# Optimization experiments

Hardware: AMD Instinct MI355X
Metric: run time of the kernel (lower is better)

Reference implementation:

```python
import jax, jax.numpy as jnp
import numpy as np
import math

B, K, T = 4, 1024, 2048
OD, H = 128, 8


def setup_inputs() -> dict:
    key = jax.random.key(0)
    ks = jax.random.split(key, 6)
    s_in = 1.0 / math.sqrt(K)
    s_u = 1.0 / math.sqrt(H * OD)
    return {
        "x": jax.random.normal(ks[0], (B, K, T), dtype=jnp.float32),
        "Wk": jax.random.uniform(ks[1], (H * OD, K), minval=-s_in, maxval=s_in, dtype=jnp.float32),
        "Wq": jax.random.uniform(ks[2], (H * OD, K), minval=-s_in, maxval=s_in, dtype=jnp.float32),
        "Wv": jax.random.uniform(ks[3], (H * OD, K), minval=-s_in, maxval=s_in, dtype=jnp.float32),
        "Wu": jax.random.uniform(ks[4], (OD, H * OD), minval=-s_u, maxval=s_u, dtype=jnp.float32),
        "bu": jax.random.uniform(ks[5], (OD,), minval=-s_u, maxval=s_u, dtype=jnp.float32),
    }


def reference(x, Wk, Wq, Wv, Wu, bu):
    b, k, t = x.shape
    # QKV projections: Linear applied over channel dim of channels-first input
    keys = jnp.einsum('bkt,jk->bjt', x, Wk).reshape(b, H, OD, t)
    queries = jnp.einsum('bkt,jk->bjt', x, Wq).reshape(b, H, OD, t)
    values = jnp.einsum('bkt,jk->bjt', x, Wv).reshape(b, H, OD, t)
    # attention scores over time: [b, h, t, t]
    dot = jnp.einsum('bhkt,bhki->bhti', queries, keys) / math.sqrt(OD)
    dot = jax.nn.softmax(dot, axis=-1)
    out = jnp.einsum('bhti,bhki->bhkt', dot, values)  # [b, h, od, t]
    # unify heads: weight (OD, H*OD) viewed as (OD_out=k, H=h, OD=e)
    out = jnp.einsum('bhet,khe->bkt', out, Wu.reshape(OD, H, OD))
    return out + bu[None, :, None]
```

## Files before the change

kernel.cpp:

```cpp
#include <hip/hip_runtime.h>
#include <hip/hip_bf16.h>
#include <type_traits>
#include <utility>

#define DEVINL __device__ __forceinline__

typedef unsigned short u16;
typedef unsigned int   u32;
typedef short  s8v  __attribute__((ext_vector_type(8)));
typedef __bf16 b8v  __attribute__((ext_vector_type(8)));
typedef float  f4v  __attribute__((ext_vector_type(4)));
typedef float  f16v __attribute__((ext_vector_type(16)));
typedef u32    u4v  __attribute__((ext_vector_type(4)));

static constexpr int BB = 4, KD = 1024, TT = 2048, OD = 128, NH = 8;
static constexpr int J2 = 2048;

template<class V, class = void> struct mfma_takes : std::false_type {};
template<class V> struct mfma_takes<V, std::void_t<decltype(
    __builtin_amdgcn_mfma_f32_16x16x32_bf16(std::declval<V>(), std::declval<V>(),
                                            std::declval<f4v>(), 0, 0, 0))>> : std::true_type {};

template<class AV>
DEVINL f4v mfma16(AV a, AV b, f4v c) {
  if constexpr (mfma_takes<AV>::value) {
    return __builtin_amdgcn_mfma_f32_16x16x32_bf16(a, b, c, 0, 0, 0);
  } else {
    return __builtin_amdgcn_mfma_f32_16x16x32_bf16(
        __builtin_bit_cast(b8v, a), __builtin_bit_cast(b8v, b), c, 0, 0, 0);
  }
}

template<class V, class = void> struct mfma32_takes : std::false_type {};
template<class V> struct mfma32_takes<V, std::void_t<decltype(
    __builtin_amdgcn_mfma_f32_32x32x16_bf16(std::declval<V>(), std::declval<V>(),
                                            std::declval<f16v>(), 0, 0, 0))>> : std::true_type {};

template<class AV>
DEVINL f16v mfma32(AV a, AV b, f16v c) {
  if constexpr (mfma32_takes<AV>::value) {
    return __builtin_amdgcn_mfma_f32_32x32x16_bf16(a, b, c, 0, 0, 0);
  } else {
    return __builtin_amdgcn_mfma_f32_32x32x16_bf16(
        __builtin_bit_cast(b8v, a), __builtin_bit_cast(b8v, b), c, 0, 0, 0);
  }
}

DEVINL u16 f2bf(float f) {
  union { float f; u32 u; } v; v.f = f;
  u32 u = v.u;
  return (u16)((u + 0x7fffu + ((u >> 16) & 1u)) >> 16);
}
DEVINL float bf2f(u16 h) { union { u32 u; float f; } v; v.u = ((u32)h) << 16; return v.f; }

DEVINL u32 cvtpk_bf16(float a, float b) {
  u32 r;
  asm("v_cvt_pk_bf16_f32 %0, %1, %2" : "=v"(r) : "v"(a), "v"(b));
  return r;
}

DEVINL void gload_lds16(const void* g, void* l) {
  __builtin_amdgcn_global_load_lds(
      (const __attribute__((address_space(1))) void*)g,
      (__attribute__((address_space(3))) void*)l, 16, 0, 0);
}

__global__ void xpose_split_x(const float* __restrict__ x, u16* __restrict__ xTh) {
  __shared__ float tile[32][33];
  const int b  = blockIdx.z;
  const int k0 = blockIdx.y * 32;
  const int t0 = blockIdx.x * 32;
  const int tx = threadIdx.x;
  const int ty = threadIdx.y;
  const float* xb = x + (size_t)b * KD * TT;
#pragma unroll
  for (int j = 0; j < 4; ++j)
    tile[ty + j * 8][tx] = xb[(size_t)(k0 + ty + j * 8) * TT + t0 + tx];
  __syncthreads();
  u16* oh = xTh + (size_t)b * TT * KD;
#pragma unroll
  for (int j = 0; j < 4; ++j) {
    int t = ty + j * 8;
    float v = tile[tx][t];
    oh[(size_t)(t0 + t) * KD + k0 + tx] = f2bf(v);
  }
}

__global__ void split_weights(const float* __restrict__ Wk, const float* __restrict__ Wq,
                              const float* __restrict__ Wv, const float* __restrict__ Wu,
                              u16* __restrict__ Wkqh, u16* __restrict__ Wvh,
                              u16* __restrict__ Wuh,  u16* __restrict__ Wul,
                              float qscale) {
  int i = blockIdx.x * 256 + threadIdx.x;
  if (i < 1048576) {
    Wkqh[i] = f2bf(Wk[i]);
    Wkqh[1048576 + i] = f2bf(Wq[i] * qscale);
    Wvh[i] = f2bf(Wv[i]);
    if (i < 131072) {
      float v = Wu[i];  u16 hh = f2bf(v);
      Wuh[i] = hh;      Wul[i] = f2bf(v - bf2f(hh));
    }
  }
}

template<int EPI>
__global__ __launch_bounds__(256, 3) void gemm_bt_split(
    const u16* __restrict__ Ahi, const u16* __restrict__ Alo,
    const u16* __restrict__ Bhi, const u16* __restrict__ Blo,
    void* __restrict__ Couth,
    const float* __restrict__ bias,
    int Kdim, int ldc, long strideA, long strideB, long strideC, int npass) {
  __shared__ __align__(16) u16 At[128 * 64];
  __shared__ __align__(16) u16 Bt[128 * 64];
  const int tid = threadIdx.x;
  const int w = tid >> 6, l = tid & 63;
  const int wm = w >> 1, wn = w & 1;
  const int lr = l & 15, lg = l >> 4;
  const int b = blockIdx.z;
  const u16* Ah = Ahi + (size_t)b * strideA;
  const u16* Al = Alo ? Alo + (size_t)b * strideA : nullptr;
  const u16* Bh = Bhi + (size_t)b * strideB;
  const u16* Bl = Blo ? Blo + (size_t)b * strideB : nullptr;
  const int m0 = blockIdx.x * 128;
  const int n0 = (EPI == 3) ? ((blockIdx.y & 15) * 128) : (blockIdx.y * 128);
  const int ky = (EPI == 3) ? (blockIdx.y >> 4) : 0;
  const int kspan = (EPI == 3) ? (Kdim / 2) : Kdim;
  const int kbase = ky * kspan;

  int srow[4], soff[4];
#pragma unroll
  for (int i = 0; i < 4; ++i) {
    int c = tid + i * 256;
    int row = c >> 3, q = c & 7;
    srow[i] = row;
    soff[i] = (q ^ (row & 7)) * 8;
  }

  f4v acc[4][4] = {};

  const int spi = kspan / 64;
  const int iters = npass * spi;
  for (int it = 0; it < iters; ++it) {
    const int seg = it / spi;
    const int k = kbase + (it - seg * spi) * 64;
    const u16* As = (seg == 2 || (seg == 1 && npass == 2)) ? Al : Ah;
    const u16* Bs = (seg == 1 && npass == 3) ? Bl : Bh;
#pragma unroll
    for (int i = 0; i < 4; ++i) {
      int c = tid + i * 256;
      gload_lds16(As + (size_t)(m0 + srow[i]) * Kdim + k + soff[i], (char*)At + c * 16);
      gload_lds16(Bs + (size_t)(n0 + srow[i]) * Kdim + k + soff[i], (char*)Bt + c * 16);
    }
    __syncthreads();
    __builtin_amdgcn_s_setprio(1);
#pragma unroll
    for (int kk = 0; kk < 2; ++kk) {
      const int q = kk * 4 + lg;
      s8v a[4], bb[4];
#pragma unroll
      for (int mi = 0; mi < 4; ++mi) {
        int row = wm * 64 + mi * 16 + lr;
        a[mi] = *(const s8v*)(&At[row * 64 + (q ^ (row & 7)) * 8]);
      }
#pragma unroll
      for (int ni = 0; ni < 4; ++ni) {
        int row = wn * 64 + ni * 16 + lr;
        bb[ni] = *(const s8v*)(&Bt[row * 64 + (q ^ (row & 7)) * 8]);
      }
#pragma unroll
      for (int mi = 0; mi < 4; ++mi)
#pragma unroll
        for (int ni = 0; ni < 4; ++ni)
          acc[mi][ni] = mfma16(a[mi], bb[ni], acc[mi][ni]);
    }
    __builtin_amdgcn_s_setprio(0);
    __syncthreads();
  }

  if constexpr (EPI == 2) {
    u16* Ch = (u16*)Couth + (size_t)b * strideC;
#pragma unroll
    for (int mi = 0; mi < 4; ++mi)
#pragma unroll
      for (int ni = 0; ni < 4; ++ni)
#pragma unroll
        for (int r = 0; r < 4; ++r) {
          int m = m0 + wm * 64 + mi * 16 + lg * 4 + r;
          int n = n0 + wn * 64 + ni * 16 + lr;
          Ch[(size_t)m * ldc + n] = f2bf(acc[mi][ni][r]);
        }
  } else if constexpr (EPI == 3) {
    float* C = (float*)Couth + ((size_t)ky * BB + b) * strideC;
#pragma unroll
    for (int mi = 0; mi < 4; ++mi)
#pragma unroll
      for (int ni = 0; ni < 4; ++ni)
#pragma unroll
        for (int r = 0; r < 4; ++r) {
          int m = m0 + wm * 64 + mi * 16 + lg * 4 + r;
          int n = n0 + wn * 64 + ni * 16 + lr;
          C[(size_t)m * ldc + n] = acc[mi][ni][r];
        }
  } else {
    float* C = (float*)Couth + (size_t)b * strideC;
#pragma unroll
    for (int mi = 0; mi < 4; ++mi)
#pragma unroll
      for (int ni = 0; ni < 4; ++ni)
#pragma unroll
        for (int r = 0; r < 4; ++r) {
          int m = m0 + wm * 64 + mi * 16 + lg * 4 + r;
          int n = n0 + wn * 64 + ni * 16 + lr;
          C[(size_t)m * ldc + n] = acc[mi][ni][r] + bias[m];
        }
  }
}

__global__ void addbias(const float* __restrict__ part, float* __restrict__ out,
                        const float* __restrict__ bias) {
  int i = blockIdx.x * 256 + threadIdx.x;
  f4v a = ((const f4v*)part)[i];
  f4v c = ((const f4v*)part)[i + 262144];
  float bs = bias[(i >> 9) & 127];
  f4v r;
#pragma unroll
  for (int j = 0; j < 4; ++j) r[j] = a[j] + c[j] + bs;
  ((f4v*)out)[i] = r;
}

__global__ __launch_bounds__(256, 2) void attn_fwd(
    const u16* __restrict__ QKTh, const u16* __restrict__ Vh,
    u16* __restrict__ OTh) {
  __shared__ __align__(16) u16 Ksh[2][32 * 128];
  __shared__ __align__(16) u16 Vsh[2][128 * 32];

  const int bid = blockIdx.x;
  const int lid = (bid & 7) * 64 + (bid >> 3);
  const int t0 = (lid & 15) * 128;
  const int h  = (lid >> 4) & 7;
  const int b  = lid >> 7;

  const int tid = threadIdx.x;
  const int w = tid >> 6, l = tid & 63;
  const int lw = l & 31, hi = l >> 5;
  const size_t qb = (size_t)b * TT * J2;
  const u16* Qh_ = QKTh + qb + 1024 + h * 128;
  const u16* Kh_ = QKTh + qb + h * 128;
  const u16* Vh_ = Vh + (size_t)b * 1024 * TT + (size_t)h * 128 * TT;

  int koff[2], kdo[2], voff[2], vdo[2];
#pragma unroll
  for (int i = 0; i < 2; ++i) {
    int c = tid + i * 256;
    { int row = c >> 4, q = c & 15;
      koff[i] = row * J2 + (q ^ (row & 7)) * 8;  kdo[i] = c * 16; }
    { int row = c >> 2, q = c & 3;
      voff[i] = row * TT + (q ^ ((row >> 1) & 3)) * 8;  vdo[i] = c * 16; }
  }

#define ATTN_STAGE(BSEL, I0) do {                                          \
    _Pragma("unroll")                                                      \
    for (int i_ = 0; i_ < 2; ++i_) {                                       \
      gload_lds16(Kh_ + (size_t)(I0) * J2 + koff[i_], (char*)Ksh[BSEL] + kdo[i_]); \
      gload_lds16(Vh_ + voff[i_] + (I0),              (char*)Vsh[BSEL] + vdo[i_]); \
    } } while (0)

  s8v qh[8];
  {
    const size_t trow = (size_t)(t0 + w * 32 + lw) * J2;
#pragma unroll
    for (int st = 0; st < 8; ++st)
      qh[st] = *(const s8v*)(Qh_ + trow + st * 16 + hi * 8);
  }

  f16v o[4] = {};
  float lsum = 0.f;

  ATTN_STAGE(0, 0);

  for (int it = 0; it < 64; ++it) {
    const int cur = it & 1;
    if (it + 1 < 64) {
      ATTN_STAGE(cur ^ 1, (it + 1) * 32);
      asm volatile("s_waitcnt vmcnt(4)" ::: "memory");
    } else {
      asm volatile("s_waitcnt vmcnt(0)" ::: "memory");
    }
    __builtin_amdgcn_s_barrier();

    const u16* Ks = Ksh[cur];
    const u16* Vs = Vsh[cur];
    f16v s = {};
    __builtin_amdgcn_s_setprio(1);
#pragma unroll
    for (int st = 0; st < 8; ++st) {
      s8v kf = *(const s8v*)(&Ks[lw * 128 + (((st * 2 + hi) ^ (lw & 7)) * 8)]);
      s = mfma32(kf, qh[st], s);
    }
    __builtin_amdgcn_s_setprio(0);

    u32 wp[4][2];
    float ps = 0.f;
#pragma unroll
    for (int g = 0; g < 4; ++g) {
      float e0 = exp2f(s[g * 4 + 0]);
      float e1 = exp2f(s[g * 4 + 1]);
      float e2 = exp2f(s[g * 4 + 2]);
      float e3 = exp2f(s[g * 4 + 3]);
      ps += (e0 + e1) + (e2 + e3);
      wp[g][0] = cvtpk_bf16(e0, e1);
      wp[g][1] = cvtpk_bf16(e2, e3);
    }
    lsum += ps;

    s8v pa[2];
#pragma unroll
    for (int ks = 0; ks < 2; ++ks) {
      u32 a0 = wp[2 * ks][0], b0 = wp[2 * ks + 1][0];
      u32 a1 = wp[2 * ks][1], b1 = wp[2 * ks + 1][1];
      asm volatile("v_permlane32_swap_b32 %0, %1" : "+v"(a0), "+v"(b0));
      asm volatile("v_permlane32_swap_b32 %0, %1" : "+v"(a1), "+v"(b1));
      u4v fw; fw[0] = a0; fw[1] = a1; fw[2] = b0; fw[3] = b1;
      pa[ks] = __builtin_bit_cast(s8v, fw);
    }

    __builtin_amdgcn_s_setprio(1);
#pragma unroll
    for (int ks = 0; ks < 2; ++ks) {
#pragma unroll
      for (int et = 0; et < 4; ++et) {
        const int vrow = et * 32 + lw;
        s8v vh = *(const s8v*)(&Vs[vrow * 32 +
                                   (((ks * 2 + hi) ^ ((vrow >> 1) & 3)) * 8)]);
        o[et] = mfma32(pa[ks], vh, o[et]);
      }
    }
    __builtin_amdgcn_s_setprio(0);
    if (it + 1 < 64)
      __builtin_amdgcn_s_barrier();
  }
#undef ATTN_STAGE

  lsum += __shfl_xor(lsum, 32);

  u16* oh = OTh + (size_t)b * TT * 1024;
#pragma unroll
  for (int r = 0; r < 16; ++r) {
    const int qrow = (r & 3) + 8 * (r >> 2) + 4 * hi;
    float ls = __shfl(lsum, qrow);
    float inv = 1.0f / ls;
    int t = t0 + w * 32 + qrow;
#pragma unroll
    for (int et = 0; et < 4; ++et) {
      int he = h * 128 + et * 32 + lw;
      oh[(size_t)t * 1024 + he] = f2bf(o[et][r] * inv);
    }
  }
}

extern "C" void kernel_launch(void* const* d_in, const int* in_sizes, int n_in,
                              void* d_out, int out_size, void* d_ws, size_t ws_size,
                              hipStream_t stream) {
  const float* x  = (const float*)d_in[0];
  const float* Wk = (const float*)d_in[1];
  const float* Wq = (const float*)d_in[2];
  const float* Wv = (const float*)d_in[3];
  const float* Wu = (const float*)d_in[4];
  const float* bu = (const float*)d_in[5];
  float* out = (float*)d_out;

  const size_t need_bytes = 2ull * (8388608ull + 2097152ull + 1048576ull +
                                    131072ull * 2 + 16777216ull + 8388608ull +
                                    8388608ull + 4194304ull);
  if (ws_size < need_bytes) {
    (void)hipMemsetAsync(d_out, 0, (size_t)out_size * sizeof(float), stream);
    return;
  }
  u16* p = (u16*)d_ws;
  u16* xTh = p;  p += 8388608;
  u16* Wkqh = p; p += 2097152;
  u16* Wvh = p;  p += 1048576;
  u16* Wuh = p;  p += 131072;
  u16* Wul = p;  p += 131072;
  u16* QKTh = p; p += 16777216;
  u16* Vh = p;   p += 8388608;
  u16* OTh = p;  p += 8388608;
  float* Cpart = (float*)p; p += 4194304;

  const float qscale = 0.08838834764831845f * 1.4426950408889634f;

  xpose_split_x<<<dim3(64, 32, 4), dim3(32, 8), 0, stream>>>(x, xTh);
  split_weights<<<4096, 256, 0, stream>>>(Wk, Wq, Wv, Wu, Wkqh, Wvh, Wuh, Wul, qscale);

  gemm_bt_split<2><<<dim3(16, 16, 4), 256, 0, stream>>>(
      xTh, nullptr, Wkqh, nullptr, QKTh, nullptr,
      1024, 2048, 2097152L, 0L, 4194304L, 1);
  gemm_bt_split<2><<<dim3(8, 16, 4), 256, 0, stream>>>(
      Wvh, nullptr, xTh, nullptr, Vh, nullptr,
      1024, 2048, 0L, 2097152L, 2097152L, 1);
  attn_fwd<<<dim3(512), dim3(256), 0, stream>>>(QKTh, Vh, OTh);
  gemm_bt_split<3><<<dim3(1, 32, 4), 256, 0, stream>>>(
      Wuh, Wul, OTh, nullptr, Cpart, nullptr,
      1024, 2048, 0L, 2097152L, 262144L, 2);
  addbias<<<1024, 256, 0, stream>>>(Cpart, out, bu);
}
```

Baseline: 187.0 us.

## Software-pipeline attention with 4-deep LDS ring and next-tile QK overlap

Result: no change. 188.3 us (+0.7%).

```diff
diff --git a/kernel.cpp b/kernel.cpp
--- a/kernel.cpp
+++ b/kernel.cpp
@@ -231,8 +231,8 @@
 __global__ __launch_bounds__(256, 2) void attn_fwd(
     const u16* __restrict__ QKTh, const u16* __restrict__ Vh,
     u16* __restrict__ OTh) {
-  __shared__ __align__(16) u16 Ksh[2][32 * 128];
-  __shared__ __align__(16) u16 Vsh[2][128 * 32];
+  __shared__ __align__(16) u16 Ksh[4][32 * 128];
+  __shared__ __align__(16) u16 Vsh[4][128 * 32];
 
   const int bid = blockIdx.x;
   const int lid = (bid & 7) * 64 + (bid >> 3);
@@ -265,6 +265,17 @@
       gload_lds16(Vh_ + voff[i_] + (I0),              (char*)Vsh[BSEL] + vdo[i_]); \
     } } while (0)
 
+#define ATTN_QK(SACC, BSEL) do {                                           \
+    const u16* Ks_ = Ksh[BSEL];                                            \
+    __builtin_amdgcn_s_setprio(1);                                         \
+    _Pragma("unroll")                                                      \
+    for (int st_ = 0; st_ < 8; ++st_) {                                    \
+      s8v kf_ = *(const s8v*)(&Ks_[lw * 128 + (((st_ * 2 + hi) ^ (lw & 7)) * 8)]); \
+      SACC = mfma32(kf_, qh[st_], SACC);                                   \
+    }                                                                      \
+    __builtin_amdgcn_s_setprio(0);                                         \
+  } while (0)
+
   s8v qh[8];
   {
     const size_t trow = (size_t)(t0 + w * 32 + lw) * J2;
@@ -277,36 +288,37 @@
   float lsum = 0.f;
 
   ATTN_STAGE(0, 0);
+  ATTN_STAGE(1, 32);
+  ATTN_STAGE(2, 64);
+  asm volatile("s_waitcnt vmcnt(8)" ::: "memory");
+  __builtin_amdgcn_s_barrier();
+
+  f16v s_cur = {};
+  ATTN_QK(s_cur, 0);
 
   for (int it = 0; it < 64; ++it) {
-    const int cur = it & 1;
-    if (it + 1 < 64) {
-      ATTN_STAGE(cur ^ 1, (it + 1) * 32);
+    if (it < 62) {
       asm volatile("s_waitcnt vmcnt(4)" ::: "memory");
     } else {
       asm volatile("s_waitcnt vmcnt(0)" ::: "memory");
     }
     __builtin_amdgcn_s_barrier();
 
-    const u16* Ks = Ksh[cur];
-    const u16* Vs = Vsh[cur];
-    f16v s = {};
-    __builtin_amdgcn_s_setprio(1);
-#pragma unroll
-    for (int st = 0; st < 8; ++st) {
-      s8v kf = *(const s8v*)(&Ks[lw * 128 + (((st * 2 + hi) ^ (lw & 7)) * 8)]);
-      s = mfma32(kf, qh[st], s);
-    }
-    __builtin_amdgcn_s_setprio(0);
+    if (it + 3 < 64)
+      ATTN_STAGE((it + 3) & 3, (it + 3) * 32);
+
+    f16v s_next = {};
+    if (it + 1 < 64)
+      ATTN_QK(s_next, (it + 1) & 3);
 
     u32 wp[4][2];
     float ps = 0.f;
 #pragma unroll
     for (int g = 0; g < 4; ++g) {
-      float e0 = exp2f(s[g * 4 + 0]);
-      float e1 = exp2f(s[g * 4 + 1]);
-      float e2 = exp2f(s[g * 4 + 2]);
-      float e3 = exp2f(s[g * 4 + 3]);
+      float e0 = exp2f(s_cur[g * 4 + 0]);
+      float e1 = exp2f(s_cur[g * 4 + 1]);
+      float e2 = exp2f(s_cur[g * 4 + 2]);
+      float e3 = exp2f(s_cur[g * 4 + 3]);
       ps += (e0 + e1) + (e2 + e3);
       wp[g][0] = cvtpk_bf16(e0, e1);
       wp[g][1] = cvtpk_bf16(e2, e3);
@@ -324,6 +336,7 @@
       pa[ks] = __builtin_bit_cast(s8v, fw);
     }
 
+    const u16* Vs = Vsh[it & 3];
     __builtin_amdgcn_s_setprio(1);
 #pragma unroll
     for (int ks = 0; ks < 2; ++ks) {
@@ -336,9 +349,10 @@
       }
     }
     __builtin_amdgcn_s_setprio(0);
-    if (it + 1 < 64)
-      __builtin_amdgcn_s_barrier();
-  }
+
+    s_cur = s_next;
+  }
+#undef ATTN_QK
 #undef ATTN_STAGE
 
   lsum += __shfl_xor(lsum, 32);
```
